# Kernel tuning notes

Hardware: AMD Instinct MI355X
Metric: run time of the kernel (lower is better)

The kernel has to match this reference:

```python
import jax, jax.numpy as jnp
import numpy as np

V, E, H, C = 50257, 256, 512, 16  # vocab, embed_dim, hidden_size, n_cells
B, T = 256, 128
LN_EPS = 1e-5


def setup_inputs() -> dict:
    key = jax.random.key(0)
    ks = jax.random.split(key, 16)
    s_h = 1.0 / np.sqrt(H)
    s_e = 1.0 / np.sqrt(E)
    return {
        "tokens": jax.random.randint(ks[0], (B, T), 0, V),
        "emb": jax.random.normal(ks[1], (V, E), jnp.float32) * 0.02,
        "Wproj": jax.random.normal(ks[2], (E, H), jnp.float32) * s_e,
        "bproj": jnp.zeros((H,), jnp.float32),
        "Wp": jax.random.normal(ks[3], (C, H, H), jnp.float32) * s_h,
        "bp": jnp.zeros((C, H), jnp.float32),
        "ln_g": jnp.ones((C, H), jnp.float32),
        "ln_b": jnp.zeros((C, H), jnp.float32),
        "Wih": jax.random.normal(ks[4], (C, 4 * H, H), jnp.float32) * s_h,
        "bih": jnp.zeros((C, 4 * H), jnp.float32),
        "Whh": jax.random.normal(ks[5], (C, 4 * H, H), jnp.float32) * s_h,
        "bhh": jnp.zeros((C, 4 * H), jnp.float32),
        "Wa": jax.random.normal(ks[6], (C, H, H), jnp.float32) * s_h,
        "ba": jnp.zeros((C, H), jnp.float32),
        "gate_logit": jnp.zeros((C,), jnp.float32),  # torch.tensor(0.0) per cell
    }


def _layernorm(x, g, b):
    mu = jnp.mean(x, axis=-1, keepdims=True)
    var = jnp.var(x, axis=-1, keepdims=True)
    return (x - mu) * jax.lax.rsqrt(var + LN_EPS) * g + b


def reference(tokens, emb, Wproj, bproj, Wp, bp, ln_g, ln_b,
              Wih, bih, Whh, bhh, Wa, ba, gate_logit):
    # embedding (padding_idx=0 zeroed) + projection to hidden size
    emb = emb.at[0].set(0.0)
    xs = emb[tokens] @ Wproj + bproj              # [B,T,H]
    xs = jnp.transpose(xs, (1, 0, 2))             # [T,B,H] for scan

    gate = jax.nn.sigmoid(gate_logit)[:, None, None]  # [C,1,1]

    def step(carry, x_t):
        h, c, ext = carry                          # h,c: [C,B,H], ext: [B,H]
        # input_adapter == Identity (input_size == hidden_size); external injection
        x = x_t[None] + 0.3 * ext[None]            # [C,B,H]
        # perception: Linear + ReLU + LayerNorm
        p = jax.nn.relu(jnp.einsum('cbh,chk->cbk', x, Wp) + bp[:, None, :])
        p = _layernorm(p, ln_g[:, None, :], ln_b[:, None, :])
        # LSTMCell (torch gate order i, f, g, o)
        gates = (jnp.einsum('cbh,cgh->cbg', p, Wih) + bih[:, None, :]
                 + jnp.einsum('cbh,cgh->cbg', h, Whh) + bhh[:, None, :])
        i_g, f_g, g_g, o_g = jnp.split(gates, 4, axis=-1)
        c_new = jax.nn.sigmoid(f_g) * c + jax.nn.sigmoid(i_g) * jnp.tanh(g_g)
        h_new = jax.nn.sigmoid(o_g) * jnp.tanh(c_new)
        # association + sigmoid gate
        a = jnp.tanh(jnp.einsum('cbh,chk->cbk', h_new, Wa) + ba[:, None, :])
        out = a * gate                             # [C,B,H]
        y = jnp.mean(out, axis=0)                  # aggregate cells -> [B,H]
        return (h_new, c_new, y), y

    h0 = jnp.zeros((C, B, H), xs.dtype)
    c0 = jnp.zeros((C, B, H), xs.dtype)
    ext0 = jnp.zeros((B, H), xs.dtype)
    _, ys = jax.lax.scan(step, (h0, c0, ext0), xs)  # ys: [T,B,H]
    return jnp.transpose(ys, (1, 0, 2))             # [B,T,H]
```

## Files before the change

kernel.cpp:

```cpp
#include <hip/hip_runtime.h>
#include <hip/hip_bf16.h>

#define V 50257
#define E 256
#define H 512
#define C 16
#define B 256
#define T 128

typedef _Float16 f16x8 __attribute__((ext_vector_type(8)));
typedef _Float16 f16x4 __attribute__((ext_vector_type(4)));
typedef float f32x4 __attribute__((ext_vector_type(4)));

__device__ __forceinline__ float sigm(float x) { return 1.0f / (1.0f + __expf(-x)); }

__device__ __forceinline__ void gload16(const _Float16* g, _Float16* l) {
  __builtin_amdgcn_global_load_lds((const __attribute__((address_space(1))) unsigned*)g,
                                   (__attribute__((address_space(3))) unsigned*)l, 16, 0, 0);
}

__global__ __launch_bounds__(256) void k_emb(const int* __restrict__ tokens,
                                             const float* __restrict__ emb,
                                             const float* __restrict__ Wproj,
                                             const float* __restrict__ bproj,
                                             _Float16* __restrict__ xs_h) {
  __shared__ float elds[16][256];
  const int tid = threadIdx.x;
  const int r0 = blockIdx.x * 16;
#pragma unroll
  for (int i = 0; i < 16; ++i) {
    int r = r0 + i;
    int t = r >> 8, b = r & 255;
    int tok = tokens[b * T + t];
    elds[i][tid] = (tok == 0) ? 0.0f : emb[(size_t)tok * E + tid];
  }
  __syncthreads();
  float acc0[16], acc1[16];
#pragma unroll
  for (int i = 0; i < 16; ++i) { acc0[i] = 0.0f; acc1[i] = 0.0f; }
  for (int k = 0; k < E; k += 4) {
    float w0[4], w1[4];
#pragma unroll
    for (int kk = 0; kk < 4; ++kk) {
      w0[kk] = Wproj[(k + kk) * H + tid];
      w1[kk] = Wproj[(k + kk) * H + tid + 256];
    }
#pragma unroll
    for (int i = 0; i < 16; ++i) {
      float4 e4 = *(const float4*)&elds[i][k];
      acc0[i] = fmaf(e4.x, w0[0], acc0[i]);
      acc0[i] = fmaf(e4.y, w0[1], acc0[i]);
      acc0[i] = fmaf(e4.z, w0[2], acc0[i]);
      acc0[i] = fmaf(e4.w, w0[3], acc0[i]);
      acc1[i] = fmaf(e4.x, w1[0], acc1[i]);
      acc1[i] = fmaf(e4.y, w1[1], acc1[i]);
      acc1[i] = fmaf(e4.z, w1[2], acc1[i]);
      acc1[i] = fmaf(e4.w, w1[3], acc1[i]);
    }
  }
  float bp0 = bproj[tid], bp1 = bproj[tid + 256];
#pragma unroll
  for (int i = 0; i < 16; ++i) {
    size_t r = (size_t)(r0 + i);
    xs_h[r * H + tid] = (_Float16)(acc0[i] + bp0);
    xs_h[r * H + tid + 256] = (_Float16)(acc1[i] + bp1);
  }
}

__global__ __launch_bounds__(256) void k_cvt_wg(const float* __restrict__ Wih,
                                                const float* __restrict__ Whh,
                                                _Float16* __restrict__ WgT) {
  for (size_t i4 = ((size_t)blockIdx.x * 256 + threadIdx.x) * 4; i4 < (size_t)33554432;
       i4 += (size_t)gridDim.x * 1024) {
    size_t c = i4 >> 21;
    size_t rem = i4 & 2097151;
    size_t n = rem >> 10;
    size_t k2 = rem & 1023;
    const float* src = (k2 < 512) ? (Wih + (c * 2048 + n) * 512 + k2)
                                  : (Whh + (c * 2048 + n) * 512 + (k2 - 512));
    float4 v = *(const float4*)src;
    f16x4 o;
    o[0] = (_Float16)v.x; o[1] = (_Float16)v.y; o[2] = (_Float16)v.z; o[3] = (_Float16)v.w;
    *(f16x4*)&WgT[i4] = o;
  }
}

__global__ __launch_bounds__(256) void k_cvt_tr(const float* __restrict__ W,
                                                _Float16* __restrict__ WT) {
  __shared__ float tl[64][65];
  const int tid = threadIdx.x;
  const int c = blockIdx.z;
  const int k0 = blockIdx.y * 64, n0 = blockIdx.x * 64;
  const float* Wc = W + (size_t)c * 262144;
#pragma unroll
  for (int q = 0; q < 16; ++q) {
    int idx = q * 256 + tid;
    int r = idx >> 6, cc = idx & 63;
    tl[r][cc] = Wc[(size_t)(k0 + r) * 512 + n0 + cc];
  }
  __syncthreads();
  _Float16* WTc = WT + (size_t)c * 262144;
#pragma unroll
  for (int q = 0; q < 16; ++q) {
    int idx = q * 256 + tid;
    int rr = idx >> 6, cc = idx & 63;
    WTc[(size_t)(n0 + rr) * 512 + k0 + cc] = (_Float16)tl[cc][rr];
  }
}

__global__ __launch_bounds__(256) void k_bias(const float* __restrict__ bih,
                                              const float* __restrict__ bhh,
                                              float* __restrict__ bsum) {
  int i = blockIdx.x * 256 + threadIdx.x;
  if (i < C * 4 * H) bsum[i] = bih[i] + bhh[i];
}

template <int EPI, int KK, int LDA, int LDB, int ACS, int BCS, int OLD, int BLD>
__global__ __launch_bounds__(256, 2) void k_gemm(const _Float16* __restrict__ A,
                                                 const _Float16* __restrict__ Bm,
                                                 _Float16* __restrict__ hout,
                                                 const float* __restrict__ bias,
                                                 const float* __restrict__ gl) {
  __shared__ _Float16 Asl[128 * 64];
  __shared__ _Float16 Bsl[128 * 64];
  const int tid = threadIdx.x;
  const int w = tid >> 6, l = tid & 63;
  const int c = blockIdx.z;
  const int m0 = blockIdx.y * 128, n0 = blockIdx.x * 128;
  const _Float16* Ab = A + (size_t)c * ACS + (size_t)m0 * LDA;
  const _Float16* Bb = Bm + (size_t)c * BCS + (size_t)n0 * LDB;
  f32x4 acc[4][4];
#pragma unroll
  for (int i = 0; i < 4; ++i)
#pragma unroll
    for (int j = 0; j < 4; ++j) acc[i][j] = (f32x4)0.0f;
  const int wm = (w >> 1) * 64, wn = (w & 1) * 64;
  const int srow = l >> 3, sj = l & 7;
#pragma unroll 1
  for (int kb = 0; kb < KK / 64; ++kb) {
#pragma unroll
    for (int q = 0; q < 4; ++q) {
      int r = w * 32 + q * 8 + srow;
      int gj = sj ^ (r & 7);
      gload16(Ab + (size_t)r * LDA + kb * 64 + gj * 8, &Asl[(w * 32 + q * 8) * 64]);
      gload16(Bb + (size_t)r * LDB + kb * 64 + gj * 8, &Bsl[(w * 32 + q * 8) * 64]);
    }
    __syncthreads();
#pragma unroll
    for (int s2 = 0; s2 < 2; ++s2) {
      f16x8 af[4], bf[4];
#pragma unroll
      for (int i = 0; i < 4; ++i) {
        int R = wm + i * 16 + (l & 15);
        int p = (s2 * 4 + (l >> 4)) ^ (R & 7);
        af[i] = *(const f16x8*)&Asl[R * 64 + p * 8];
        int RN = wn + i * 16 + (l & 15);
        int pn = (s2 * 4 + (l >> 4)) ^ (RN & 7);
        bf[i] = *(const f16x8*)&Bsl[RN * 64 + pn * 8];
      }
#pragma unroll
      for (int i = 0; i < 4; ++i)
#pragma unroll
        for (int j = 0; j < 4; ++j)
          acc[i][j] = __builtin_amdgcn_mfma_f32_16x16x32_f16(af[i], bf[j], acc[i][j], 0, 0, 0);
    }
    __syncthreads();
  }
  float gv = 0.0f;
  if (EPI == 2) gv = sigm(gl[c]);
  const int rl = (l >> 4) * 4, cl = l & 15;
#pragma unroll
  for (int i = 0; i < 4; ++i) {
#pragma unroll
    for (int j = 0; j < 4; ++j) {
      int gc = n0 + wn + j * 16 + cl;
      float bv = bias[(size_t)c * BLD + gc];
#pragma unroll
      for (int rg = 0; rg < 4; ++rg) {
        int gr = m0 + wm + i * 16 + rl + rg;
        float v = acc[i][j][rg] + bv;
        if (EPI == 0) v = fmaxf(v, 0.0f);
        if (EPI == 2) v = tanhf(v) * gv;
        hout[(size_t)c * (256 * (size_t)OLD) + (size_t)gr * OLD + gc] = (_Float16)v;
      }
    }
  }
}

__global__ __launch_bounds__(256) void k_ln(_Float16* __restrict__ Aq,
                                            const float* __restrict__ g,
                                            const float* __restrict__ b) {
  int row = blockIdx.x * 4 + (threadIdx.x >> 6);
  int l = threadIdx.x & 63;
  int c = row >> 8;
  _Float16* p = Aq + (size_t)row * 1024 + l * 8;
  f16x8 v = *(const f16x8*)p;
  float vf[8];
  float s1 = 0.0f, s2 = 0.0f;
#pragma unroll
  for (int j = 0; j < 8; ++j) {
    vf[j] = (float)v[j];
    s1 += vf[j];
    s2 += vf[j] * vf[j];
  }
#pragma unroll
  for (int m = 1; m < 64; m <<= 1) {
    s1 += __shfl_xor(s1, m, 64);
    s2 += __shfl_xor(s2, m, 64);
  }
  float mu = s1 * (1.0f / 512.0f);
  float var = s2 * (1.0f / 512.0f) - mu * mu;
  float rs = rsqrtf(var + 1e-5f);
  int col0 = l * 8;
#pragma unroll
  for (int j = 0; j < 8; ++j) {
    float o = (vf[j] - mu) * rs * g[c * 512 + col0 + j] + b[c * 512 + col0 + j];
    v[j] = (_Float16)o;
  }
  *(f16x8*)p = v;
}

__global__ __launch_bounds__(256) void k_lstm(const _Float16* __restrict__ gq,
                                              float* __restrict__ cbuf,
                                              _Float16* __restrict__ Aq) {
  int idx = blockIdx.x * 256 + threadIdx.x;
  int c = idx >> 15, rem = idx & 32767;
  int b = rem >> 7, h4 = (rem & 127) << 2;
  const _Float16* Gr = gq + ((size_t)c * 256 + b) * 2048;
  f16x4 ig4 = *(const f16x4*)&Gr[h4];
  f16x4 fg4 = *(const f16x4*)&Gr[512 + h4];
  f16x4 gg4 = *(const f16x4*)&Gr[1024 + h4];
  f16x4 og4 = *(const f16x4*)&Gr[1536 + h4];
  float4 cv = *(float4*)&cbuf[(size_t)idx * 4];
  float* cvp = &cv.x;
  f16x4 hh;
#pragma unroll
  for (int j = 0; j < 4; ++j) {
    float cn = sigm((float)fg4[j]) * cvp[j] + sigm((float)ig4[j]) * tanhf((float)gg4[j]);
    cvp[j] = cn;
    hh[j] = (_Float16)(sigm((float)og4[j]) * tanhf(cn));
  }
  *(float4*)&cbuf[(size_t)idx * 4] = cv;
  *(f16x4*)&Aq[((size_t)c * 256 + b) * 1024 + 512 + h4] = hh;
}

__global__ __launch_bounds__(256) void k_agg(const _Float16* __restrict__ abuf,
                                             const _Float16* __restrict__ xs_h,
                                             _Float16* __restrict__ xq,
                                             float* __restrict__ out, int t) {
  int idx = blockIdx.x * 256 + threadIdx.x;
  int i4 = idx * 4;
  float s[4] = {0.0f, 0.0f, 0.0f, 0.0f};
#pragma unroll
  for (int c = 0; c < 16; ++c) {
    f16x4 a = *(const f16x4*)&abuf[(size_t)c * 131072 + i4];
#pragma unroll
    for (int j = 0; j < 4; ++j) s[j] += (float)a[j];
  }
  int b = i4 >> 9, h = i4 & 511;
  float4 y4;
  float* yp = &y4.x;
#pragma unroll
  for (int j = 0; j < 4; ++j) yp[j] = s[j] * (1.0f / 16.0f);
  *(float4*)&out[((size_t)b * T + t) * 512 + h] = y4;
  if (t + 1 < T) {
    f16x4 xs4 = *(const f16x4*)&xs_h[(size_t)(t + 1) * 131072 + i4];
    f16x4 xn;
#pragma unroll
    for (int j = 0; j < 4; ++j) xn[j] = (_Float16)((float)xs4[j] + 0.3f * yp[j]);
    *(f16x4*)&xq[i4] = xn;
  }
}

extern "C" void kernel_launch(void* const* d_in, const int* in_sizes, int n_in,
                              void* d_out, int out_size, void* d_ws, size_t ws_size,
                              hipStream_t stream) {
  const int* tokens = (const int*)d_in[0];
  const float* emb = (const float*)d_in[1];
  const float* Wproj = (const float*)d_in[2];
  const float* bproj = (const float*)d_in[3];
  const float* Wp = (const float*)d_in[4];
  const float* bp = (const float*)d_in[5];
  const float* ln_g = (const float*)d_in[6];
  const float* ln_b = (const float*)d_in[7];
  const float* Wih = (const float*)d_in[8];
  const float* bih = (const float*)d_in[9];
  const float* Whh = (const float*)d_in[10];
  const float* bhh = (const float*)d_in[11];
  const float* Wa = (const float*)d_in[12];
  const float* ba = (const float*)d_in[13];
  const float* gl = (const float*)d_in[14];
  float* out = (float*)d_out;

  char* w8 = (char*)d_ws;
  _Float16* xs_h = (_Float16*)w8;
  _Float16* Aq = (_Float16*)(w8 + 33554432);
  _Float16* gatesq = (_Float16*)(w8 + 50331648);
  float* cbuf = (float*)(w8 + 67108864);
  _Float16* abuf = (_Float16*)(w8 + 75497472);
  _Float16* xq = (_Float16*)(w8 + 79691776);
  _Float16* WpT = (_Float16*)(w8 + 79953920);
  _Float16* WaT = (_Float16*)(w8 + 88342528);
  _Float16* WgT = (_Float16*)(w8 + 96731136);
  float* bsum = (float*)(w8 + 163840000);

  hipMemsetAsync(Aq, 0, 16777216, stream);
  hipMemsetAsync(cbuf, 0, 8388608, stream);

  k_cvt_wg<<<4096, 256, 0, stream>>>(Wih, Whh, WgT);
  k_cvt_tr<<<dim3(8, 8, 16), 256, 0, stream>>>(Wp, WpT);
  k_cvt_tr<<<dim3(8, 8, 16), 256, 0, stream>>>(Wa, WaT);
  k_bias<<<128, 256, 0, stream>>>(bih, bhh, bsum);
  k_emb<<<T * B / 16, 256, 0, stream>>>(tokens, emb, Wproj, bproj, xs_h);
  hipMemcpyAsync(xq, xs_h, 262144, hipMemcpyDeviceToDevice, stream);

  for (int t = 0; t < T; ++t) {
    k_gemm<0, 512, 512, 512, 0, 262144, 1024, 512>
        <<<dim3(4, 2, 16), 256, 0, stream>>>(xq, WpT, Aq, bp, nullptr);
    k_ln<<<1024, 256, 0, stream>>>(Aq, ln_g, ln_b);
    k_gemm<1, 1024, 1024, 1024, 262144, 2097152, 2048, 2048>
        <<<dim3(16, 2, 16), 256, 0, stream>>>(Aq, WgT, gatesq, bsum, nullptr);
    k_lstm<<<2048, 256, 0, stream>>>(gatesq, cbuf, Aq);
    k_gemm<2, 512, 1024, 512, 262144, 262144, 512, 512>
        <<<dim3(4, 2, 16), 256, 0, stream>>>(Aq + 512, WaT, abuf, ba, gl);
    k_agg<<<128, 256, 0, stream>>>(abuf, xs_h, xq, out, t);
  }
}
```

Measured before the change: 8.628 ms.

## Fuse LSTM cell update into gate GEMM epilogue with interleaved gate weights

Reorders the concatenated gate weight rows and summed bias so each 64-column warp tile holds the i, f, g and o gates for the same 16 hidden units. The LSTM state update then runs in the gate GEMM epilogue, which removes the separate k_lstm kernel and the fp16 gates buffer round trip. The A operand is double-buffered (Ac/An) so the GEMM can write the new h without racing against blocks still reading the old h. In exchange, the epilogue does scattered scalar cell-state loads and stores and heavier transcendental work per thread.

```diff
diff --git a/kernel.cpp b/kernel.cpp
--- a/kernel.cpp
+++ b/kernel.cpp
@@ -74,8 +74,11 @@
        i4 += (size_t)gridDim.x * 1024) {
     size_t c = i4 >> 21;
     size_t rem = i4 & 2097151;
-    size_t n = rem >> 10;
+    size_t np = rem >> 10;
     size_t k2 = rem & 1023;
+    int gate = (int)((np >> 4) & 3);
+    int hh = (int)(((np >> 6) << 4) | (np & 15));
+    size_t n = (size_t)gate * 512 + hh;
     const float* src = (k2 < 512) ? (Wih + (c * 2048 + n) * 512 + k2)
                                   : (Whh + (c * 2048 + n) * 512 + (k2 - 512));
     float4 v = *(const float4*)src;
@@ -112,7 +115,13 @@
                                               const float* __restrict__ bhh,
                                               float* __restrict__ bsum) {
   int i = blockIdx.x * 256 + threadIdx.x;
-  if (i < C * 4 * H) bsum[i] = bih[i] + bhh[i];
+  if (i < C * 4 * H) {
+    int c = i >> 11, np = i & 2047;
+    int gate = (np >> 4) & 3;
+    int hh = ((np >> 6) << 4) | (np & 15);
+    int n = gate * 512 + hh;
+    bsum[i] = bih[c * 2048 + n] + bhh[c * 2048 + n];
+  }
 }
 
 template <int EPI, int KK, int LDA, int LDB, int ACS, int BCS, int OLD, int BLD>
@@ -120,7 +129,9 @@
                                                  const _Float16* __restrict__ Bm,
                                                  _Float16* __restrict__ hout,
                                                  const float* __restrict__ bias,
-                                                 const float* __restrict__ gl) {
+                                                 const float* __restrict__ gl,
+                                                 float* __restrict__ cstate,
+                                                 _Float16* __restrict__ hdst) {
   __shared__ _Float16 Asl[128 * 64];
   __shared__ _Float16 Bsl[128 * 64];
   const int tid = threadIdx.x;
@@ -166,22 +177,44 @@
     }
     __syncthreads();
   }
-  float gv = 0.0f;
-  if (EPI == 2) gv = sigm(gl[c]);
   const int rl = (l >> 4) * 4, cl = l & 15;
-#pragma unroll
-  for (int i = 0; i < 4; ++i) {
-#pragma unroll
-    for (int j = 0; j < 4; ++j) {
-      int gc = n0 + wn + j * 16 + cl;
-      float bv = bias[(size_t)c * BLD + gc];
+  if (EPI == 3) {
+    const int hh = (((n0 + wn) >> 6) << 4) + cl;
+    float bv[4];
+#pragma unroll
+    for (int j = 0; j < 4; ++j) bv[j] = bias[(size_t)c * BLD + (n0 + wn) + j * 16 + cl];
+#pragma unroll
+    for (int i = 0; i < 4; ++i) {
 #pragma unroll
       for (int rg = 0; rg < 4; ++rg) {
-        int gr = m0 + wm + i * 16 + rl + rg;
-        float v = acc[i][j][rg] + bv;
-        if (EPI == 0) v = fmaxf(v, 0.0f);
-        if (EPI == 2) v = tanhf(v) * gv;
-        hout[(size_t)c * (256 * (size_t)OLD) + (size_t)gr * OLD + gc] = (_Float16)v;
+        int row = m0 + wm + i * 16 + rl + rg;
+        float ig = acc[i][0][rg] + bv[0];
+        float fg = acc[i][1][rg] + bv[1];
+        float gg = acc[i][2][rg] + bv[2];
+        float og = acc[i][3][rg] + bv[3];
+        size_t ci = ((size_t)c * 256 + row) * 512 + hh;
+        float cn = sigm(fg) * cstate[ci] + sigm(ig) * tanhf(gg);
+        cstate[ci] = cn;
+        hdst[((size_t)c * 256 + row) * 1024 + 512 + hh] = (_Float16)(sigm(og) * tanhf(cn));
+      }
+    }
+  } else {
+    float gv = 0.0f;
+    if (EPI == 2) gv = sigm(gl[c]);
+#pragma unroll
+    for (int i = 0; i < 4; ++i) {
+#pragma unroll
+      for (int j = 0; j < 4; ++j) {
+        int gc = n0 + wn + j * 16 + cl;
+        float bv = bias[(size_t)c * BLD + gc];
+#pragma unroll
+        for (int rg = 0; rg < 4; ++rg) {
+          int gr = m0 + wm + i * 16 + rl + rg;
+          float v = acc[i][j][rg] + bv;
+          if (EPI == 0) v = fmaxf(v, 0.0f);
+          if (EPI == 2) v = tanhf(v) * gv;
+          hout[(size_t)c * (256 * (size_t)OLD) + (size_t)gr * OLD + gc] = (_Float16)v;
+        }
       }
     }
   }
@@ -218,30 +251,6 @@
     v[j] = (_Float16)o;
   }
   *(f16x8*)p = v;
-}
-
-__global__ __launch_bounds__(256) void k_lstm(const _Float16* __restrict__ gq,
-                                              float* __restrict__ cbuf,
-                                              _Float16* __restrict__ Aq) {
-  int idx = blockIdx.x * 256 + threadIdx.x;
-  int c = idx >> 15, rem = idx & 32767;
-  int b = rem >> 7, h4 = (rem & 127) << 2;
-  const _Float16* Gr = gq + ((size_t)c * 256 + b) * 2048;
-  f16x4 ig4 = *(const f16x4*)&Gr[h4];
-  f16x4 fg4 = *(const f16x4*)&Gr[512 + h4];
-  f16x4 gg4 = *(const f16x4*)&Gr[1024 + h4];
-  f16x4 og4 = *(const f16x4*)&Gr[1536 + h4];
-  float4 cv = *(float4*)&cbuf[(size_t)idx * 4];
-  float* cvp = &cv.x;
-  f16x4 hh;
-#pragma unroll
-  for (int j = 0; j < 4; ++j) {
-    float cn = sigm((float)fg4[j]) * cvp[j] + sigm((float)ig4[j]) * tanhf((float)gg4[j]);
-    cvp[j] = cn;
-    hh[j] = (_Float16)(sigm((float)og4[j]) * tanhf(cn));
-  }
-  *(float4*)&cbuf[(size_t)idx * 4] = cv;
-  *(f16x4*)&Aq[((size_t)c * 256 + b) * 1024 + 512 + h4] = hh;
 }
 
 __global__ __launch_bounds__(256) void k_agg(const _Float16* __restrict__ abuf,
@@ -294,8 +303,8 @@
 
   char* w8 = (char*)d_ws;
   _Float16* xs_h = (_Float16*)w8;
-  _Float16* Aq = (_Float16*)(w8 + 33554432);
-  _Float16* gatesq = (_Float16*)(w8 + 50331648);
+  _Float16* Aq0 = (_Float16*)(w8 + 33554432);
+  _Float16* Aq1 = (_Float16*)(w8 + 50331648);
   float* cbuf = (float*)(w8 + 67108864);
   _Float16* abuf = (_Float16*)(w8 + 75497472);
   _Float16* xq = (_Float16*)(w8 + 79691776);
@@ -304,7 +313,7 @@
   _Float16* WgT = (_Float16*)(w8 + 96731136);
   float* bsum = (float*)(w8 + 163840000);
 
-  hipMemsetAsync(Aq, 0, 16777216, stream);
+  hipMemsetAsync(Aq0, 0, 16777216, stream);
   hipMemsetAsync(cbuf, 0, 8388608, stream);
 
   k_cvt_wg<<<4096, 256, 0, stream>>>(Wih, Whh, WgT);
@@ -315,14 +324,15 @@
   hipMemcpyAsync(xq, xs_h, 262144, hipMemcpyDeviceToDevice, stream);
 
   for (int t = 0; t < T; ++t) {
+    _Float16* Ac = (t & 1) ? Aq1 : Aq0;
+    _Float16* An = (t & 1) ? Aq0 : Aq1;
     k_gemm<0, 512, 512, 512, 0, 262144, 1024, 512>
-        <<<dim3(4, 2, 16), 256, 0, stream>>>(xq, WpT, Aq, bp, nullptr);
-    k_ln<<<1024, 256, 0, stream>>>(Aq, ln_g, ln_b);
-    k_gemm<1, 1024, 1024, 1024, 262144, 2097152, 2048, 2048>
-        <<<dim3(16, 2, 16), 256, 0, stream>>>(Aq, WgT, gatesq, bsum, nullptr);
-    k_lstm<<<2048, 256, 0, stream>>>(gatesq, cbuf, Aq);
+        <<<dim3(4, 2, 16), 256, 0, stream>>>(xq, WpT, Ac, bp, nullptr, nullptr, nullptr);
+    k_ln<<<1024, 256, 0, stream>>>(Ac, ln_g, ln_b);
+    k_gemm<3, 1024, 1024, 1024, 262144, 2097152, 1, 2048>
+        <<<dim3(16, 2, 16), 256, 0, stream>>>(Ac, WgT, nullptr, bsum, nullptr, cbuf, An);
     k_gemm<2, 512, 1024, 512, 262144, 262144, 512, 512>
-        <<<dim3(4, 2, 16), 256, 0, stream>>>(Aq + 512, WaT, abuf, ba, gl);
+        <<<dim3(4, 2, 16), 256, 0, stream>>>(An + 512, WaT, abuf, ba, gl, nullptr, nullptr);
     k_agg<<<128, 256, 0, stream>>>(abuf, xs_h, xq, out, t);
   }
 }
```

Result: faster. 7.975 ms (-7.6%).
